# Performance work log

Measured on AMD Instinct MI355X. Metric: run time of the kernel, lower is better.

Reference implementation:

```python
import jax, jax.numpy as jnp
import numpy as np

B, L = 8, 512
EMB, NHEAD, HD = 512, 8, 64
FFN, NL = 2048, 6
VOCAB, NRE, RING_START, PAD, MAXLEN = 45, 20, 24, 0, 512
NOUT0 = VOCAB - NRE  # 25
NEG = -jnp.inf


def _ln(x, g, b, eps=1e-5):
    m = jnp.mean(x, -1, keepdims=True)
    v = jnp.mean((x - m) ** 2, -1, keepdims=True)
    return (x - m) * jax.lax.rsqrt(v + eps) * g + b


def setup_inputs():
    key = jax.random.key(0)
    ks = jax.random.split(key, 24)
    p = lambda k, shape: jax.random.normal(k, shape, jnp.float32) * 0.02
    return {
        "sequences": jax.random.randint(ks[0], (B, L), 1, VOCAB),  # avoid PAD=0
        "count_sequences": jax.random.randint(ks[1], (B, L), 0, MAXLEN),
        "graph_mask_sequences": jax.random.bernoulli(ks[2], 0.05, (B, L, VOCAB)),
        "valence_mask_sequences": jax.random.bernoulli(ks[3], 0.05, (B, L, VOCAB)),
        "linear_loc_squares": jax.random.randint(ks[4], (B, L, L), 0, MAXLEN + 1),
        "up_loc_squares": jax.random.randint(ks[5], (B, L, L), 0, MAXLEN + 1),
        "down_loc_squares": jax.random.randint(ks[6], (B, L, L), 0, MAXLEN + 1),
        "tok_emb": p(ks[7], (VOCAB, EMB)),
        "cnt_emb": p(ks[8], (MAXLEN, EMB)),
        "lin_loc_emb": p(ks[9], (MAXLEN + 1, NHEAD)),
        "up_loc_emb": p(ks[10], (MAXLEN + 1, NHEAD)),
        "down_loc_emb": p(ks[11], (MAXLEN + 1, NHEAD)),
        "in_proj_w": p(ks[12], (NL, 3 * EMB, EMB)),
        "in_proj_b": jnp.zeros((NL, 3 * EMB), jnp.float32),
        "out_w": p(ks[13], (NL, EMB, EMB)),
        "out_b": jnp.zeros((NL, EMB), jnp.float32),
        "ln1_g": jnp.ones((NL, EMB), jnp.float32),
        "ln1_b": jnp.zeros((NL, EMB), jnp.float32),
        "ln2_g": jnp.ones((NL, EMB), jnp.float32),
        "ln2_b": jnp.zeros((NL, EMB), jnp.float32),
        "ffn_w1": p(ks[14], (NL, FFN, EMB)),
        "ffn_b1": jnp.zeros((NL, FFN), jnp.float32),
        "ffn_w2": p(ks[15], (NL, EMB, FFN)),
        "ffn_b2": jnp.zeros((NL, EMB), jnp.float32),
        "fin_g": jnp.ones((EMB,), jnp.float32),
        "fin_b": jnp.zeros((EMB,), jnp.float32),
        "gen_w": p(ks[16], (NOUT0, EMB)),
        "gen_b": jnp.zeros((NOUT0,), jnp.float32),
        "ring_w0": p(ks[17], (EMB, EMB)),
        "ring_b0": jnp.zeros((EMB,), jnp.float32),
        "ring_w1": p(ks[18], (EMB, EMB)),
        "ring_b1": jnp.zeros((EMB,), jnp.float32),
    }


def _forward(tok_emb, cnt_emb, lin_loc_emb, up_loc_emb, down_loc_emb,
             in_proj_w, in_proj_b, out_w, out_b, ln1_g, ln1_b, ln2_g, ln2_b,
             ffn_w1, ffn_b1, ffn_w2, ffn_b2, fin_g, fin_b, gen_w, gen_b,
             ring_w0, ring_b0, ring_w1, ring_b1,
             sequences, count_sequences, graph_mask_sequences,
             valence_mask_sequences, linear_loc_squares, up_loc_squares,
             down_loc_squares):
    scale_e = jnp.sqrt(jnp.float32(EMB))
    x = tok_emb[sequences] * scale_e + cnt_emb[count_sequences] * scale_e  # (B,L,E)

    # per-head additive attention bias from three (B,L,L) index lookups
    bias = lin_loc_emb[linear_loc_squares] + up_loc_emb[up_loc_squares] + down_loc_emb[down_loc_squares]  # (B,L,L,H)
    bias = jnp.transpose(bias, (0, 3, 1, 2))  # (B,H,Lq,Lk)
    causal = jnp.tril(jnp.ones((L, L), bool))
    attn_bias = jnp.where(causal[None, None], bias, NEG)
    pad = sequences == PAD  # key padding
    attn_bias = jnp.where(pad[:, None, None, :], NEG, attn_bias)

    inv_sqrt_hd = 1.0 / jnp.sqrt(jnp.float32(HD))
    for i in range(NL):  # post-norm TransformerEncoderLayer, gelu
        qkv = jnp.einsum('ble,fe->blf', x, in_proj_w[i]) + in_proj_b[i]
        q, k, v = jnp.split(qkv, 3, axis=-1)
        q = q.reshape(B, L, NHEAD, HD)
        k = k.reshape(B, L, NHEAD, HD)
        v = v.reshape(B, L, NHEAD, HD)
        scores = jnp.einsum('bqhd,bkhd->bhqk', q, k) * inv_sqrt_hd + attn_bias
        a = jax.nn.softmax(scores, axis=-1)
        ctx = jnp.einsum('bhqk,bkhd->bqhd', a, v).reshape(B, L, EMB)
        attn_out = jnp.einsum('ble,fe->blf', ctx, out_w[i]) + out_b[i]
        x = _ln(x + attn_out, ln1_g[i], ln1_b[i])
        h = jax.nn.gelu(jnp.einsum('ble,fe->blf', x, ffn_w1[i]) + ffn_b1[i], approximate=False)
        ff = jnp.einsum('blf,ef->ble', h, ffn_w2[i]) + ffn_b2[i]
        x = _ln(x + ff, ln2_g[i], ln2_b[i])
    x = _ln(x, fin_g, fin_b)

    logits0 = jnp.einsum('ble,oe->blo', x, gen_w) + gen_b  # (B,L,NOUT0)

    # EdgeLogitLayer: scatter ring-start projections into NRE slots
    out0 = jnp.einsum('ble,he->blh', x, ring_w0) + ring_b0
    out1_ = jnp.einsum('ble,he->blh', x, ring_w1) + ring_b1
    ring_start = sequences == RING_START
    idx = jnp.where(ring_start, jnp.cumsum(ring_start.astype(jnp.int32), axis=1), 0)  # (B,L)
    bidx = jnp.arange(B)[:, None]
    slots = jnp.zeros((B, NRE + 1, EMB), x.dtype).at[bidx, idx].set(out1_, mode='drop')
    ring_tab = slots[:, 1:]  # drop slot 0 (non-ring-start writes)
    logits1 = jnp.einsum('ble,bre->blr', out0, ring_tab) * (EMB ** -0.5)

    logits = jnp.concatenate([logits0, logits1], axis=2)  # (B,L,VOCAB)
    logits = jnp.where(graph_mask_sequences, NEG, logits)
    logits = jnp.where(valence_mask_sequences, NEG, logits)
    return logits


def reference(sequences, count_sequences, graph_mask_sequences, valence_mask_sequences,
              linear_loc_squares, up_loc_squares, down_loc_squares,
              tok_emb, cnt_emb, lin_loc_emb, up_loc_emb, down_loc_emb,
              in_proj_w, in_proj_b, out_w, out_b, ln1_g, ln1_b, ln2_g, ln2_b,
              ffn_w1, ffn_b1, ffn_w2, ffn_b2, fin_g, fin_b, gen_w, gen_b,
              ring_w0, ring_b0, ring_w1, ring_b1):
    return _forward(tok_emb, cnt_emb, lin_loc_emb, up_loc_emb, down_loc_emb,
                    in_proj_w, in_proj_b, out_w, out_b, ln1_g, ln1_b, ln2_g, ln2_b,
                    ffn_w1, ffn_b1, ffn_w2, ffn_b2, fin_g, fin_b, gen_w, gen_b,
                    ring_w0, ring_b0, ring_w1, ring_b1,
                    sequences, count_sequences, graph_mask_sequences,
                    valence_mask_sequences, linear_loc_squares, up_loc_squares,
                    down_loc_squares)
```

## Files before the change

kernel.cpp:

```cpp
#include <hip/hip_runtime.h>
#include <cmath>

#define BB 8
#define LL 512
#define EMB 512
#define NHEAD 8
#define HD 64
#define FFN 2048
#define NL 6
#define VOCAB 45
#define NRE 20
#define RING_START 24
#define NOUT0 25
#define BL 4096

#define BIG_NEG -1.0e30f

typedef __bf16 bf16x8 __attribute__((ext_vector_type(8)));
typedef __bf16 bf16x4 __attribute__((ext_vector_type(4)));
typedef float f32x4 __attribute__((ext_vector_type(4)));

__device__ __forceinline__ void ld_g2l(const __bf16* g, __bf16* l) {
  __builtin_amdgcn_global_load_lds(
      (const __attribute__((address_space(1))) unsigned int*)g,
      (__attribute__((address_space(3))) unsigned int*)l, 16, 0, 0);
}

__global__ __launch_bounds__(256) void megacast_kernel(
    const float* __restrict__ s0, const float* __restrict__ s1,
    const float* __restrict__ s2, const float* __restrict__ s3,
    const float* __restrict__ s4, const float* __restrict__ s5,
    const float* __restrict__ s6, const float* __restrict__ s7,
    const float* __restrict__ s8, __bf16* __restrict__ dw,
    __bf16* __restrict__ dt) {
  const int gid = blockIdx.x * 256 + threadIdx.x;
  const int szs[9] = {589824, 196608, 786432, 786432, 32768,
                      32768,  513,    513,    513};
  const float* srcs[9] = {s0, s1, s2, s3, s4, s5, s6, s7, s8};
  int seg = 0, base = 0;
  while (seg < 9 && gid >= base + szs[seg]) { base += szs[seg]; seg++; }
  if (seg >= 9) return;
  const int local = gid - base;
  const float* src = srcs[seg];
  const float4 a = ((const float4*)src)[local * 2];
  const float4 b = ((const float4*)src)[local * 2 + 1];
  bf16x8 v;
  v[0] = (__bf16)a.x; v[1] = (__bf16)a.y; v[2] = (__bf16)a.z; v[3] = (__bf16)a.w;
  v[4] = (__bf16)b.x; v[5] = (__bf16)b.y; v[6] = (__bf16)b.z; v[7] = (__bf16)b.w;
  __bf16* dst = (seg < 6) ? (dw + (size_t)base * 8 + (size_t)local * 8)
                          : (dt + (size_t)(seg - 6) * 4104 + (size_t)local * 8);
  *(bf16x8*)dst = v;
}

__global__ __launch_bounds__(128) void embed_kernel(
    const int* __restrict__ seq, const int* __restrict__ cnt,
    const float* __restrict__ tok_emb, const float* __restrict__ cnt_emb,
    float* __restrict__ x, __bf16* __restrict__ xb) {
  const int row = blockIdx.x;
  const int t = seq[row];
  const int c = cnt[row];
  const float scale = 22.627416997969522f;
  const int j = threadIdx.x * 4;
  float4 tv = *(const float4*)(tok_emb + (size_t)t * EMB + j);
  float4 cv = *(const float4*)(cnt_emb + (size_t)c * EMB + j);
  float4 o;
  o.x = (tv.x + cv.x) * scale;
  o.y = (tv.y + cv.y) * scale;
  o.z = (tv.z + cv.z) * scale;
  o.w = (tv.w + cv.w) * scale;
  *(float4*)(x + (size_t)row * EMB + j) = o;
  bf16x4 h;
  h[0] = (__bf16)o.x; h[1] = (__bf16)o.y; h[2] = (__bf16)o.z; h[3] = (__bf16)o.w;
  *(bf16x4*)(xb + (size_t)row * EMB + j) = h;
}

__global__ __launch_bounds__(256) void bias_kernel(
    const int* __restrict__ lin_sq, const int* __restrict__ up_sq,
    const int* __restrict__ down_sq,
    const __bf16* __restrict__ tl16, const __bf16* __restrict__ tu16,
    const __bf16* __restrict__ td16,
    const int* __restrict__ seq, __bf16* __restrict__ bias) {
  __shared__ __bf16 Tl[513 * 8], Tu[513 * 8], Td[513 * 8];
  __shared__ int seqs[LL];
  const int tid = threadIdx.x;
  const int b = blockIdx.x >> 6;
  const int q0 = (blockIdx.x & 63) * 8;
  for (int i = tid; i < 513; i += 256) {
    *(bf16x8*)&Tl[i * 8] = *(const bf16x8*)&tl16[i * 8];
    *(bf16x8*)&Tu[i * 8] = *(const bf16x8*)&tu16[i * 8];
    *(bf16x8*)&Td[i * 8] = *(const bf16x8*)&td16[i * 8];
  }
  for (int i = tid; i < LL; i += 256) seqs[i] = seq[b * LL + i];
  __syncthreads();
  for (int q = q0; q < q0 + 8; q++) {
    const size_t rbase = ((size_t)(b * LL + q)) * LL;
    for (int k = tid; k <= q; k += 256) {
      const int li = lin_sq[rbase + k], ui = up_sq[rbase + k],
                di = down_sq[rbase + k];
      const bool valid = (seqs[k] != 0);
      bf16x8 a = *(const bf16x8*)&Tl[li * 8];
      bf16x8 u = *(const bf16x8*)&Tu[ui * 8];
      bf16x8 d = *(const bf16x8*)&Td[di * 8];
#pragma unroll
      for (int h = 0; h < NHEAD; h++) {
        float v = valid ? ((float)a[h] + (float)u[h] + (float)d[h])
                        : -INFINITY;
        bias[(((size_t)(b * NHEAD + h) * LL) + q) * LL + k] = (__bf16)v;
      }
    }
  }
}

template <int BM, int BN, int ACT, int OUTBF, int RES, int SPLITK, int B2>
__global__ __launch_bounds__(256) void gemm_mfma_kernel(
    const __bf16* __restrict__ A, const __bf16* __restrict__ W,
    const float* __restrict__ bias, const float* __restrict__ bias2,
    float* __restrict__ C, __bf16* __restrict__ Cb,
    const float* __restrict__ Res, int N, int K, int lda) {
  constexpr int MI = BM / 32;
  constexpr int NI = BN / 32;
  __shared__ __bf16 As[BM * 32];
  __shared__ __bf16 Ws[BN * 32];
  const int tid = threadIdx.x;
  const int lane = tid & 63, wave = tid >> 6;
  const int wm = wave >> 1, wn = wave & 1;
  const int q = lane >> 4, l15 = lane & 15;
  const int m0 = blockIdx.y * BM, n0 = blockIdx.x * BN;
  const int kz = SPLITK ? blockIdx.z : 0;

  const __bf16* Ag =
      A + (size_t)(m0 + (tid >> 2)) * lda + (tid & 3) * 8 + (size_t)kz * K;
  const __bf16* Wg =
      W + (size_t)(n0 + (tid >> 2)) * lda + (tid & 3) * 8 + (size_t)kz * K;
  __bf16* Al = &As[tid * 8];
  __bf16* Wl = &Ws[tid * 8];

  f32x4 acc[MI][NI] = {};

  for (int k0 = 0; k0 < K; k0 += 32) {
    ld_g2l(Ag + k0, Al);
    if (BM == 128) ld_g2l(Ag + k0 + (size_t)64 * lda, Al + 2048);
    ld_g2l(Wg + k0, Wl);
    if (BN == 128) ld_g2l(Wg + k0 + (size_t)64 * lda, Wl + 2048);
    __syncthreads();
    bf16x8 af[MI], bfr[NI];
#pragma unroll
    for (int mi = 0; mi < MI; mi++)
      af[mi] =
          *(const bf16x8*)&As[(wm * (BM / 2) + mi * 16 + l15) * 32 + q * 8];
#pragma unroll
    for (int ni = 0; ni < NI; ni++)
      bfr[ni] =
          *(const bf16x8*)&Ws[(wn * (BN / 2) + ni * 16 + l15) * 32 + q * 8];
#pragma unroll
    for (int mi = 0; mi < MI; mi++)
#pragma unroll
      for (int ni = 0; ni < NI; ni++)
        acc[mi][ni] = __builtin_amdgcn_mfma_f32_16x16x32_bf16(
            af[mi], bfr[ni], acc[mi][ni], 0, 0, 0);
    __syncthreads();
  }

  float* Cz = SPLITK ? (C + (size_t)kz * ((size_t)BL * N)) : C;
#pragma unroll
  for (int ni = 0; ni < NI; ni++) {
    const int n = n0 + wn * (BN / 2) + ni * 16 + l15;
    float bv = 0.f;
    if (!SPLITK || kz == 0)
      bv = (B2 && n >= EMB) ? bias2[n - EMB] : bias[n];
#pragma unroll
    for (int mi = 0; mi < MI; mi++) {
#pragma unroll
      for (int r = 0; r < 4; r++) {
        const int m = m0 + wm * (BM / 2) + mi * 16 + q * 4 + r;
        float v = acc[mi][ni][r] + bv;
        if (RES && (!SPLITK || kz == 0)) v += Res[(size_t)m * N + n];
        if (ACT == 1) v = 0.5f * v * (1.0f + erff(v * 0.70710678118654752f));
        if (OUTBF)
          Cb[(size_t)m * N + n] = (__bf16)v;
        else
          Cz[(size_t)m * N + n] = v;
      }
    }
  }
}

__global__ __launch_bounds__(256) void attn_fused_kernel(
    const __bf16* __restrict__ qkv, const __bf16* __restrict__ bias,
    __bf16* __restrict__ ctx) {
  __shared__ __bf16 Ks[64][72];
  __shared__ __bf16 Vt[64][72];
  __shared__ __bf16 Ps[64][72];
  const int tid = threadIdx.x;
  const int lane = tid & 63, w = tid >> 6;
  const int q = lane >> 4, l15 = lane & 15;
  int id = blockIdx.x;
  int bh, qt;
  if (id < 256) { bh = id >> 2; qt = 7 - (id & 3); }
  else { id -= 256; bh = id >> 2; qt = id & 3; }
  const int b = bh >> 3, h = bh & 7;
  const int q0 = qt * 64;
  const float inv_sqrt_hd = 0.125f;

  const int srow = tid >> 2, c0 = (tid & 3) * 16;
  {
    const __bf16* qsrc =
        qkv + (size_t)(b * LL + q0 + srow) * 1536 + h * HD + c0;
    *(bf16x8*)&Ps[srow][c0] = *(const bf16x8*)qsrc;
    *(bf16x8*)&Ps[srow][c0 + 8] = *(const bf16x8*)(qsrc + 8);
  }
  __syncthreads();
  const bf16x8 aq0 = *(const bf16x8*)&Ps[w * 16 + l15][q * 8];
  const bf16x8 aq1 = *(const bf16x8*)&Ps[w * 16 + l15][32 + q * 8];

  f32x4 o4[4] = {};
  float m[4], l[4];
#pragma unroll
  for (int r = 0; r < 4; r++) { m[r] = -INFINITY; l[r] = 0.f; }

  for (int kt = 0; kt <= qt; kt++) {
    const int k0 = kt * 64;
    __syncthreads();
    {
      const __bf16* src = qkv + (size_t)(b * LL + k0 + srow) * 1536 + h * HD;
      bf16x8 kv0 = *(const bf16x8*)(src + 512 + c0);
      bf16x8 kv1 = *(const bf16x8*)(src + 512 + c0 + 8);
      bf16x8 vv0 = *(const bf16x8*)(src + 1024 + c0);
      bf16x8 vv1 = *(const bf16x8*)(src + 1024 + c0 + 8);
      *(bf16x8*)&Ks[srow][c0] = kv0;
      *(bf16x8*)&Ks[srow][c0 + 8] = kv1;
#pragma unroll
      for (int j = 0; j < 8; j++) {
        Vt[c0 + j][srow] = vv0[j];
        Vt[c0 + 8 + j][srow] = vv1[j];
      }
    }
    __syncthreads();

    f32x4 s4[4] = {};
#pragma unroll
    for (int ni = 0; ni < 4; ni++) {
      bf16x8 bk0 = *(const bf16x8*)&Ks[ni * 16 + l15][q * 8];
      bf16x8 bk1 = *(const bf16x8*)&Ks[ni * 16 + l15][32 + q * 8];
      s4[ni] =
          __builtin_amdgcn_mfma_f32_16x16x32_bf16(aq0, bk0, s4[ni], 0, 0, 0);
      s4[ni] =
          __builtin_amdgcn_mfma_f32_16x16x32_bf16(aq1, bk1, s4[ni], 0, 0, 0);
    }

    const bool diag = (kt == qt);
    const size_t bbase = ((size_t)bh * LL + (q0 + w * 16 + q * 4)) * LL + k0;
#pragma unroll
    for (int r = 0; r < 4; r++) {
      const int qrow = w * 16 + q * 4 + r;
      float sv[4];
#pragma unroll
      for (int ni = 0; ni < 4; ni++) {
        sv[ni] = s4[ni][r] * inv_sqrt_hd +
                 (float)bias[bbase + (size_t)r * LL + ni * 16 + l15];
        if (diag && (ni * 16 + l15 > qrow)) sv[ni] = -INFINITY;
      }
      float tm = fmaxf(fmaxf(sv[0], sv[1]), fmaxf(sv[2], sv[3]));
#pragma unroll
      for (int off = 1; off < 16; off <<= 1)
        tm = fmaxf(tm, __shfl_xor(tm, off, 16));
      const float mnew = fmaxf(m[r], tm);
      const float alpha = expf(m[r] - mnew);
      float rs = 0.f;
#pragma unroll
      for (int ni = 0; ni < 4; ni++) {
        const float p = expf(sv[ni] - mnew);
        Ps[qrow][ni * 16 + l15] = (__bf16)p;
        rs += p;
      }
#pragma unroll
      for (int off = 1; off < 16; off <<= 1) rs += __shfl_xor(rs, off, 16);
      l[r] = l[r] * alpha + rs;
      m[r] = mnew;
#pragma unroll
      for (int ni = 0; ni < 4; ni++) o4[ni][r] *= alpha;
    }
    __syncthreads();

    {
      bf16x8 ap0 = *(const bf16x8*)&Ps[w * 16 + l15][q * 8];
      bf16x8 ap1 = *(const bf16x8*)&Ps[w * 16 + l15][32 + q * 8];
#pragma unroll
      for (int ni = 0; ni < 4; ni++) {
        bf16x8 bv0 = *(const bf16x8*)&Vt[ni * 16 + l15][q * 8];
        bf16x8 bv1 = *(const bf16x8*)&Vt[ni * 16 + l15][32 + q * 8];
        o4[ni] =
            __builtin_amdgcn_mfma_f32_16x16x32_bf16(ap0, bv0, o4[ni], 0, 0, 0);
        o4[ni] =
            __builtin_amdgcn_mfma_f32_16x16x32_bf16(ap1, bv1, o4[ni], 0, 0, 0);
      }
    }
  }

#pragma unroll
  for (int r = 0; r < 4; r++) {
    const int qrow = w * 16 + q * 4 + r;
    const float inv = 1.0f / l[r];
    __bf16* dst = ctx + (size_t)(b * LL + q0 + qrow) * EMB + h * HD + l15;
#pragma unroll
    for (int ni = 0; ni < 4; ni++) dst[ni * 16] = (__bf16)(o4[ni][r] * inv);
  }
}

template <int NSUM>
__global__ __launch_bounds__(256) void add_ln_kernel(
    const float* __restrict__ xin, const float* __restrict__ g,
    const float* __restrict__ bta, float* __restrict__ out,
    __bf16* __restrict__ outb) {
  const int row = blockIdx.x;
  const int tid = threadIdx.x;
  float v0 = 0.f, v1 = 0.f;
#pragma unroll
  for (int sId = 0; sId < NSUM; sId++) {
    const float* xr = xin + (size_t)sId * BL * EMB + (size_t)row * EMB;
    v0 += xr[tid * 2];
    v1 += xr[tid * 2 + 1];
  }
  float s = v0 + v1, ss = v0 * v0 + v1 * v1;
#pragma unroll
  for (int off = 1; off < 64; off <<= 1) {
    s += __shfl_xor(s, off, 64);
    ss += __shfl_xor(ss, off, 64);
  }
  __shared__ float sbuf[8];
  const int wave = tid >> 6, lane = tid & 63;
  if (lane == 0) { sbuf[wave] = s; sbuf[4 + wave] = ss; }
  __syncthreads();
  s = sbuf[0] + sbuf[1] + sbuf[2] + sbuf[3];
  ss = sbuf[4] + sbuf[5] + sbuf[6] + sbuf[7];
  const float mean = s * (1.0f / EMB);
  const float var = ss * (1.0f / EMB) - mean * mean;
  const float rstd = rsqrtf(var + 1e-5f);
  const float o0 = (v0 - mean) * rstd * g[tid * 2] + bta[tid * 2];
  const float o1 = (v1 - mean) * rstd * g[tid * 2 + 1] + bta[tid * 2 + 1];
  float* orow = out + (size_t)row * EMB;
  orow[tid * 2] = o0;
  orow[tid * 2 + 1] = o1;
  if (outb) {
    __bf16* brow = outb + (size_t)row * EMB;
    brow[tid * 2] = (__bf16)o0;
    brow[tid * 2 + 1] = (__bf16)o1;
  }
}

__global__ __launch_bounds__(256) void ring_scatter_kernel(
    const int* __restrict__ seq, const float* __restrict__ o01,
    float* __restrict__ ring_tab) {
  const int b = blockIdx.x;
  const int tid = threadIdx.x;
  float* rt = ring_tab + (size_t)b * NRE * EMB;
  for (int i = tid; i < NRE * EMB; i += 256) rt[i] = 0.f;
  __shared__ int pos[NRE];
  __shared__ int cntr;
  if (tid == 0) {
    int c = 0;
    for (int l = 0; l < LL; l++) {
      if (seq[b * LL + l] == RING_START) {
        c++;
        if (c <= NRE) pos[c - 1] = l;
      }
    }
    cntr = (c < NRE) ? c : NRE;
  }
  __syncthreads();
  const int n = cntr;
  for (int r = 0; r < n; r++) {
    const float* src = o01 + (size_t)(b * LL + pos[r]) * 1024 + 512;
    for (int i = tid; i < EMB; i += 256) rt[r * EMB + i] = src[i];
  }
}

__global__ __launch_bounds__(256) void head_kernel(
    const float* __restrict__ xf, const float* __restrict__ o01,
    const float* __restrict__ ring_tab, const float* __restrict__ gen_w,
    const float* __restrict__ gen_b, const int* __restrict__ gmask,
    const int* __restrict__ vmask, float* __restrict__ out) {
  const int row = blockIdx.x;
  const int b = row >> 9;
  const int tid = threadIdx.x;
  __shared__ float xr[EMB], o0s[EMB];
  {
    float2 a = ((const float2*)(xf + (size_t)row * EMB))[tid];
    ((float2*)xr)[tid] = a;
    float2 c = ((const float2*)(o01 + (size_t)row * 1024))[tid];
    ((float2*)o0s)[tid] = c;
  }
  __syncthreads();
  const int wave = tid >> 6, lane = tid & 63;
  for (int o = wave; o < VOCAB; o += 4) {
    const float* wrow;
    const float* src;
    float bv, scale;
    if (o < NOUT0) {
      wrow = gen_w + (size_t)o * EMB;
      bv = gen_b[o];
      src = xr;
      scale = 1.0f;
    } else {
      wrow = ring_tab + ((size_t)b * NRE + (o - NOUT0)) * EMB;
      bv = 0.0f;
      src = o0s;
      scale = 0.044194173824159216f;
    }
    float sum = 0.f;
#pragma unroll
    for (int j = 0; j < 8; j++) {
      const int d = lane + 64 * j;
      sum += src[d] * wrow[d];
    }
#pragma unroll
    for (int off = 1; off < 64; off <<= 1) sum += __shfl_xor(sum, off, 64);
    if (lane == 0) {
      float v = sum * scale + bv;
      const size_t oidx = (size_t)row * VOCAB + o;
      if (gmask[oidx] != 0 || vmask[oidx] != 0) v = BIG_NEG;
      out[oidx] = v;
    }
  }
}

extern "C" void kernel_launch(void* const* d_in, const int* in_sizes, int n_in,
                              void* d_out, int out_size, void* d_ws,
                              size_t ws_size, hipStream_t stream) {
  const int* seq = (const int*)d_in[0];
  const int* cnt = (const int*)d_in[1];
  const int* gmask = (const int*)d_in[2];
  const int* vmask = (const int*)d_in[3];
  const int* lin_sq = (const int*)d_in[4];
  const int* up_sq = (const int*)d_in[5];
  const int* down_sq = (const int*)d_in[6];
  const float* tok_emb = (const float*)d_in[7];
  const float* cnt_emb = (const float*)d_in[8];
  const float* lin_e = (const float*)d_in[9];
  const float* up_e = (const float*)d_in[10];
  const float* down_e = (const float*)d_in[11];
  const float* in_proj_w = (const float*)d_in[12];
  const float* in_proj_b = (const float*)d_in[13];
  const float* out_w = (const float*)d_in[14];
  const float* out_b = (const float*)d_in[15];
  const float* ln1_g = (const float*)d_in[16];
  const float* ln1_b = (const float*)d_in[17];
  const float* ln2_g = (const float*)d_in[18];
  const float* ln2_b = (const float*)d_in[19];
  const float* ffn_w1 = (const float*)d_in[20];
  const float* ffn_b1 = (const float*)d_in[21];
  const float* ffn_w2 = (const float*)d_in[22];
  const float* ffn_b2 = (const float*)d_in[23];
  const float* fin_g = (const float*)d_in[24];
  const float* fin_b = (const float*)d_in[25];
  const float* gen_w = (const float*)d_in[26];
  const float* gen_b = (const float*)d_in[27];
  const float* ring_w0 = (const float*)d_in[28];
  const float* ring_b0 = (const float*)d_in[29];
  const float* ring_w1 = (const float*)d_in[30];
  const float* ring_b1 = (const float*)d_in[31];

  char* p = (char*)d_ws;
  auto alloc_f = [&](size_t n) { float* r = (float*)p; p += n * 4; return r; };
  auto alloc_h = [&](size_t n) { __bf16* r = (__bf16*)p; p += n * 2; return r; };

  float* x = alloc_f((size_t)BL * EMB);
  float* pbuf = alloc_f((size_t)BL * EMB);
  float* xfb = alloc_f((size_t)BL * EMB);
  float* o01b = alloc_f((size_t)BL * 1024);
  float* ringb = alloc_f((size_t)BB * NRE * EMB);
  __bf16* biasb = alloc_h((size_t)BB * NHEAD * LL * LL);
  __bf16* xb = alloc_h((size_t)BL * EMB);
  __bf16* qkvb16 = alloc_h((size_t)BL * 3 * EMB);
  __bf16* ctxb = alloc_h((size_t)BL * EMB);
  __bf16* hb = alloc_h((size_t)BL * FFN);
  __bf16* xfb16 = alloc_h((size_t)BL * EMB);
  __bf16* wqkv = alloc_h((size_t)NL * 3 * EMB * EMB);
  __bf16* wout = alloc_h((size_t)NL * EMB * EMB);
  __bf16* wf1 = alloc_h((size_t)NL * FFN * EMB);
  __bf16* wf2 = alloc_h((size_t)NL * EMB * FFN);
  __bf16* wr01 = alloc_h((size_t)2 * EMB * EMB);
  __bf16* tl16 = hb;
  __bf16* tu16 = hb + 4104;
  __bf16* td16 = hb + 8208;

  megacast_kernel<<<9478, 256, 0, stream>>>(
      in_proj_w, out_w, ffn_w1, ffn_w2, ring_w0, ring_w1, lin_e, up_e, down_e,
      wqkv, tl16);

  embed_kernel<<<BL, 128, 0, stream>>>(seq, cnt, tok_emb, cnt_emb, x, xb);
  bias_kernel<<<BB * 64, 256, 0, stream>>>(lin_sq, up_sq, down_sq, tl16, tu16,
                                           td16, seq, biasb);

  for (int i = 0; i < NL; i++) {
    gemm_mfma_kernel<64, 128, 0, 1, 0, 0, 0><<<dim3(12, 64), 256, 0, stream>>>(
        xb, wqkv + (size_t)i * 3 * EMB * EMB, in_proj_b + (size_t)i * 3 * EMB,
        nullptr, nullptr, qkvb16, nullptr, 3 * EMB, EMB, EMB);
    attn_fused_kernel<<<512, 256, 0, stream>>>(qkvb16, biasb, ctxb);
    gemm_mfma_kernel<64, 64, 0, 0, 1, 0, 0><<<dim3(8, 64), 256, 0, stream>>>(
        ctxb, wout + (size_t)i * EMB * EMB, out_b + (size_t)i * EMB, nullptr,
        pbuf, nullptr, x, EMB, EMB, EMB);
    add_ln_kernel<1><<<BL, 256, 0, stream>>>(
        pbuf, ln1_g + (size_t)i * EMB, ln1_b + (size_t)i * EMB, x, xb);
    gemm_mfma_kernel<64, 128, 1, 1, 0, 0, 0><<<dim3(16, 64), 256, 0, stream>>>(
        xb, wf1 + (size_t)i * FFN * EMB, ffn_b1 + (size_t)i * FFN, nullptr,
        nullptr, hb, nullptr, FFN, EMB, EMB);
    gemm_mfma_kernel<64, 64, 0, 0, 1, 0, 0><<<dim3(8, 64), 256, 0, stream>>>(
        hb, wf2 + (size_t)i * EMB * FFN, ffn_b2 + (size_t)i * EMB, nullptr,
        pbuf, nullptr, x, EMB, FFN, FFN);
    add_ln_kernel<1><<<BL, 256, 0, stream>>>(
        pbuf, ln2_g + (size_t)i * EMB, ln2_b + (size_t)i * EMB, x, xb);
  }

  add_ln_kernel<1><<<BL, 256, 0, stream>>>(x, fin_g, fin_b, xfb, xfb16);
  gemm_mfma_kernel<64, 128, 0, 0, 0, 0, 1><<<dim3(8, 64), 256, 0, stream>>>(
      xfb16, wr01, ring_b0, ring_b1, o01b, nullptr, nullptr, 1024, EMB, EMB);
  ring_scatter_kernel<<<BB, 256, 0, stream>>>(seq, o01b, ringb);
  head_kernel<<<BL, 256, 0, stream>>>(xfb, o01b, ringb, gen_w, gen_b, gmask,
                                      vmask, (float*)d_out);
}
```

Measured before the change: 1.073 ms.

## Split causal attention across key chunks with separate combine kernel

```diff
diff --git a/kernel.cpp b/kernel.cpp
--- a/kernel.cpp
+++ b/kernel.cpp
@@ -185,21 +185,23 @@
   }
 }
 
-__global__ __launch_bounds__(256) void attn_fused_kernel(
+__global__ __launch_bounds__(256) void attn_tile2_kernel(
     const __bf16* __restrict__ qkv, const __bf16* __restrict__ bias,
-    __bf16* __restrict__ ctx) {
+    __bf16* __restrict__ Po, float2* __restrict__ Pml) {
   __shared__ __bf16 Ks[64][72];
   __shared__ __bf16 Vt[64][72];
   __shared__ __bf16 Ps[64][72];
   const int tid = threadIdx.x;
   const int lane = tid & 63, w = tid >> 6;
   const int q = lane >> 4, l15 = lane & 15;
-  int id = blockIdx.x;
-  int bh, qt;
-  if (id < 256) { bh = id >> 2; qt = 7 - (id & 3); }
-  else { id -= 256; bh = id >> 2; qt = id & 3; }
+  const int bh = blockIdx.y;
   const int b = bh >> 3, h = bh & 7;
+  const int pidx = blockIdx.x;
+  int qt = 0, acc0 = 0;
+  while (acc0 + (qt / 2 + 1) <= pidx) { acc0 += qt / 2 + 1; qt++; }
+  const int j = pidx - acc0;
   const int q0 = qt * 64;
+  const int slot = (bh * 8 + qt) * 4 + j;
   const float inv_sqrt_hd = 0.125f;
 
   const int srow = tid >> 2, c0 = (tid & 3) * 16;
@@ -218,7 +220,8 @@
 #pragma unroll
   for (int r = 0; r < 4; r++) { m[r] = -INFINITY; l[r] = 0.f; }
 
-  for (int kt = 0; kt <= qt; kt++) {
+  const int ktEnd = (2 * j + 1 <= qt) ? (2 * j + 1) : qt;
+  for (int kt = 2 * j; kt <= ktEnd; kt++) {
     const int k0 = kt * 64;
     __syncthreads();
     {
@@ -230,9 +233,9 @@
       *(bf16x8*)&Ks[srow][c0] = kv0;
       *(bf16x8*)&Ks[srow][c0 + 8] = kv1;
 #pragma unroll
-      for (int j = 0; j < 8; j++) {
-        Vt[c0 + j][srow] = vv0[j];
-        Vt[c0 + 8 + j][srow] = vv1[j];
+      for (int jj = 0; jj < 8; jj++) {
+        Vt[c0 + jj][srow] = vv0[jj];
+        Vt[c0 + 8 + jj][srow] = vv1[jj];
       }
     }
     __syncthreads();
@@ -300,11 +303,62 @@
 #pragma unroll
   for (int r = 0; r < 4; r++) {
     const int qrow = w * 16 + q * 4 + r;
-    const float inv = 1.0f / l[r];
-    __bf16* dst = ctx + (size_t)(b * LL + q0 + qrow) * EMB + h * HD + l15;
-#pragma unroll
-    for (int ni = 0; ni < 4; ni++) dst[ni * 16] = (__bf16)(o4[ni][r] * inv);
-  }
+    if (l15 == 0)
+      Pml[(size_t)slot * 64 + qrow] = make_float2(m[r], l[r]);
+    __bf16* dst = Po + (size_t)slot * 4096 + qrow * 64 + l15;
+#pragma unroll
+    for (int ni = 0; ni < 4; ni++) dst[ni * 16] = (__bf16)o4[ni][r];
+  }
+}
+
+__global__ __launch_bounds__(256) void attn_combine_kernel(
+    const __bf16* __restrict__ Po, const float2* __restrict__ Pml,
+    __bf16* __restrict__ ctx) {
+  const int tid = threadIdx.x;
+  const int bh = blockIdx.x >> 3;
+  const int qt = blockIdx.x & 7;
+  const int b = bh >> 3, h = bh & 7;
+  const int nsl = qt / 2 + 1;
+  const int slot0 = blockIdx.x * 4;
+  __shared__ float wls[4][64];
+  __shared__ float invl[64];
+  if (tid < 64) {
+    float mg = -3.0e38f;
+    for (int s = 0; s < nsl; s++)
+      mg = fmaxf(mg, Pml[(size_t)(slot0 + s) * 64 + tid].x);
+    float lsum = 0.f;
+    for (int s = 0; s < nsl; s++) {
+      const float2 ml = Pml[(size_t)(slot0 + s) * 64 + tid];
+      const float wk = expf(ml.x - mg);
+      wls[s][tid] = wk;
+      lsum += ml.y * wk;
+    }
+    invl[tid] = 1.0f / lsum;
+  }
+  __syncthreads();
+  const int row = tid >> 2, d0 = (tid & 3) * 16;
+  float acc[16] = {};
+  for (int s = 0; s < nsl; s++) {
+    const __bf16* src = Po + (size_t)(slot0 + s) * 4096 + row * 64 + d0;
+    const float wk = wls[s][row];
+    bf16x8 v0 = *(const bf16x8*)src;
+    bf16x8 v1 = *(const bf16x8*)(src + 8);
+#pragma unroll
+    for (int jj = 0; jj < 8; jj++) {
+      acc[jj] += (float)v0[jj] * wk;
+      acc[8 + jj] += (float)v1[jj] * wk;
+    }
+  }
+  const float il = invl[row];
+  bf16x8 o0, o1;
+#pragma unroll
+  for (int jj = 0; jj < 8; jj++) {
+    o0[jj] = (__bf16)(acc[jj] * il);
+    o1[jj] = (__bf16)(acc[8 + jj] * il);
+  }
+  __bf16* dst = ctx + (size_t)(b * LL + qt * 64 + row) * EMB + h * HD + d0;
+  *(bf16x8*)dst = o0;
+  *(bf16x8*)(dst + 8) = o1;
 }
 
 template <int NSUM>
@@ -469,6 +523,8 @@
   float* xfb = alloc_f((size_t)BL * EMB);
   float* o01b = alloc_f((size_t)BL * 1024);
   float* ringb = alloc_f((size_t)BB * NRE * EMB);
+  float2* attn_pml = (float2*)alloc_f((size_t)2048 * 64 * 2);
+  __bf16* attn_po = alloc_h((size_t)2048 * 4096);
   __bf16* biasb = alloc_h((size_t)BB * NHEAD * LL * LL);
   __bf16* xb = alloc_h((size_t)BL * EMB);
   __bf16* qkvb16 = alloc_h((size_t)BL * 3 * EMB);
@@ -496,7 +552,9 @@
     gemm_mfma_kernel<64, 128, 0, 1, 0, 0, 0><<<dim3(12, 64), 256, 0, stream>>>(
         xb, wqkv + (size_t)i * 3 * EMB * EMB, in_proj_b + (size_t)i * 3 * EMB,
         nullptr, nullptr, qkvb16, nullptr, 3 * EMB, EMB, EMB);
-    attn_fused_kernel<<<512, 256, 0, stream>>>(qkvb16, biasb, ctxb);
+    attn_tile2_kernel<<<dim3(20, 64), 256, 0, stream>>>(qkvb16, biasb, attn_po,
+                                                        attn_pml);
+    attn_combine_kernel<<<512, 256, 0, stream>>>(attn_po, attn_pml, ctxb);
     gemm_mfma_kernel<64, 64, 0, 0, 1, 0, 0><<<dim3(8, 64), 256, 0, stream>>>(
         ctxb, wout + (size_t)i * EMB * EMB, out_b + (size_t)i * EMB, nullptr,
         pbuf, nullptr, x, EMB, EMB, EMB);
```

Measured after the change: 993.1 us. 7.4% less time.
